# Kernel tuning notes

Measured on AMD Instinct MI355X. Metric: run time of the kernel, lower is better.

## Reference

```python
import jax, jax.numpy as jnp
import numpy as np
from jax import lax

# dims
B, H, W, C = 32, 64, 64, 256
FEATURES, HEADS, NQ = 256, 8, 2
K, STRIDE, PAD = 3, 2, 1
HD = FEATURES // HEADS  # head dim = 32


def setup_inputs() -> dict:
    key = jax.random.key(0)
    ks = jax.random.split(key, 7)
    x = jax.random.normal(ks[0], (B, H, W, C), jnp.float32)
    # learned shared queries: truncated normal * sqrt(1/head_dim)
    query = jax.random.truncated_normal(ks[1], -2.0, 2.0, (NQ, FEATURES), jnp.float32) * np.float32(np.sqrt(1.0 / HD))
    Wk = jax.random.normal(ks[2], (C, FEATURES), jnp.float32) * np.float32(np.sqrt(1.0 / C))  # lecun
    Wv = jax.random.normal(ks[3], (C, FEATURES), jnp.float32) * np.float32(np.sqrt(1.0 / C))
    rpe_bias = jax.random.truncated_normal(ks[4], -2.0, 2.0, (K * K, NQ * HEADS), jnp.float32) * np.float32(0.02)
    attn_scale_w = jax.random.normal(ks[5], (K * K, NQ * HEADS), jnp.float32) * np.float32(0.02)
    Wo = jax.random.normal(ks[6], (FEATURES, FEATURES), jnp.float32) * np.float32(np.sqrt(1.0 / FEATURES))
    return {"x": x, "query": query, "Wk": Wk, "Wv": Wv,
            "rpe_bias": rpe_bias, "attn_scale_w": attn_scale_w, "Wo": Wo}


def _qna_forward(x, query, Wk, Wv, rpe_bias, attn_scale_w, Wo):
    # --- queries: reshape to [NQ, HEADS, HD], unit-normalize per head, depth-scale ---
    q = query.reshape(NQ, HEADS, HD)
    q = q / (jnp.linalg.norm(q, axis=-1, keepdims=True) + 1e-6)
    q = q / jnp.sqrt(HD).astype(q.dtype)

    # --- fused QK: (q Wk^T) applied to x, never materializing per-window keys ---
    Wk_r = Wk.reshape(C, HEADS, HD)
    qWk = jnp.einsum('qHd,DHd->DqH', q, Wk_r)              # [C, NQ, HEADS]
    cost = jnp.einsum('bijD,DqH->bijqH', x, qWk)            # [B, H, W, NQ, HEADS]
    cost_exp = jnp.exp(cost - lax.stop_gradient(jnp.max(cost)))  # global shift, cancels in softmax

    # --- values ---
    v = jnp.einsum('bijD,DF->bijF', x, Wv)                  # [B, H, W, FEATURES]
    v_cost_exp = cost_exp[..., None] * v.reshape(B, H, W, 1, HEADS, HD)
    v_cost_exp = v_cost_exp.reshape(B, H, W, NQ * FEATURES)

    # --- relative position bias + per-offset query mixing scale ---
    rpe = rpe_bias.reshape(K, K, 1, NQ * HEADS)
    rpe_exp = jnp.exp(rpe - lax.stop_gradient(jnp.max(rpe)))  # shift cancels (appears in num & den)
    scale = attn_scale_w.reshape(K, K, 1, NQ * HEADS)
    num_kernel = jnp.repeat(rpe_exp * scale, HD, axis=-1)   # [K, K, 1, NQ*FEATURES]

    # numerator: windowed sum of exp(cost)*v weighted by exp(rpe)*scale (depthwise conv)
    num = lax.conv_general_dilated(
        v_cost_exp, num_kernel, window_strides=(STRIDE, STRIDE),
        padding=((PAD, PAD), (PAD, PAD)), feature_group_count=NQ * FEATURES,
        dimension_numbers=('NHWC', 'HWIO', 'NHWC'))
    # denominator: windowed sum of exp(cost) weighted by exp(rpe)
    den = lax.conv_general_dilated(
        cost_exp.reshape(B, H, W, NQ * HEADS), rpe_exp, window_strides=(STRIDE, STRIDE),
        padding=((PAD, PAD), (PAD, PAD)), feature_group_count=NQ * HEADS,
        dimension_numbers=('NHWC', 'HWIO', 'NHWC'))
    ho, wo = num.shape[1], num.shape[2]

    out = num.reshape(B, ho, wo, NQ, HEADS, HD) / den.reshape(B, ho, wo, NQ, HEADS, 1)
    out = out.sum(axis=3).reshape(B, ho, wo, FEATURES)      # combine queries
    return jnp.einsum('bijF,FO->bijO', out, Wo)             # output projection


def reference(x, query, Wk, Wv, rpe_bias, attn_scale_w, Wo):
    return _qna_forward(x, query, Wk, Wv, rpe_bias, attn_scale_w, Wo)
```

## Files before the change

kernel.cpp:

```cpp
#include <hip/hip_runtime.h>
#include <math.h>

typedef __attribute__((ext_vector_type(8))) short bf16x8;
typedef __attribute__((ext_vector_type(4))) float floatx4;

static __device__ __forceinline__ short f2bf(float f) {
    union { float f; unsigned u; } a; a.f = f;
    unsigned r = a.u + 0x7fffu + ((a.u >> 16) & 1u);
    return (short)(r >> 16);
}
static __device__ __forceinline__ float bf2f(short s) {
    union { unsigned u; float f; } c; c.u = ((unsigned)(unsigned short)s) << 16;
    return c.f;
}

__global__ __launch_bounds__(256) void prep_kernel(
    const float* __restrict__ query,
    const float* __restrict__ Wk,
    const float* __restrict__ rpe_bias,
    const float* __restrict__ attn_scale_w,
    float* __restrict__ qwk,
    float* __restrict__ rpe_exp,
    float* __restrict__ rpe_scale)
{
    __shared__ float qn[16 * 33];
    __shared__ float Wt[16][260];
    int tid = threadIdx.x, bb = blockIdx.x;

    for (int i = tid; i < 512; i += 256) {
        int qq  = i >> 8;
        int rem = i & 255;
        int h   = rem >> 5;
        int d   = rem & 31;
        qn[((qq << 3) + h) * 33 + d] = query[i];
    }
    for (int i = tid; i < 16 * 256; i += 256)
        Wt[i >> 8][i & 255] = Wk[bb * 16 * 256 + i];
    __syncthreads();
    if (tid < 16) {
        float s = 0.f;
        #pragma unroll
        for (int d = 0; d < 32; ++d) { float t = qn[tid * 33 + d]; s += t * t; }
        float inv = 1.0f / ((sqrtf(s) + 1e-6f) * sqrtf(32.0f));
        #pragma unroll
        for (int d = 0; d < 32; ++d) qn[tid * 33 + d] *= inv;
    }
    __syncthreads();

    int g  = tid & 15;
    int Dl = tid >> 4;
    int h2 = g & 7;
    float acc = 0.f;
    #pragma unroll
    for (int d = 0; d < 32; ++d)
        acc += qn[g * 33 + d] * Wt[Dl][h2 * 32 + d];
    qwk[(bb * 16 + Dl) * 16 + g] = acc;

    if (bb == 0 && tid < 144) {
        float r = expf(rpe_bias[tid]);
        rpe_exp[tid]   = r;
        rpe_scale[tid] = r * attn_scale_w[tid];
    }
}

__global__ __launch_bounds__(256) void pack_kernel(
    const float* __restrict__ qwk, const float* __restrict__ Wv,
    const float* __restrict__ Wo,
    short* __restrict__ Bq, short* __restrict__ Wvh, short* __restrict__ Bo)
{
    int id = blockIdx.x * 256 + threadIdx.x;
    if (id < 4096) {
        int j = id & 7, lane = (id >> 3) & 63, kc = id >> 9;
        int k = kc * 32 + ((lane >> 4) << 3) + j;
        Bq[id] = f2bf(qwk[k * 16 + (lane & 15)]);
    } else if (id < 69632) {
        int id1 = id - 4096;
        int j = id1 & 7, lane = (id1 >> 3) & 63, kc = (id1 >> 9) & 7;
        int nt = (id1 >> 12) & 1, h = id1 >> 13;
        int k = kc * 32 + ((lane >> 4) << 3) + j;
        int n = h * 32 + nt * 16 + (lane & 15);
        Wvh[id1] = f2bf(Wv[k * 256 + n]);
    } else {
        int id2 = id - 69632;
        int j = id2 & 7, lane = (id2 >> 3) & 63, kc = (id2 >> 9) & 7, nt = id2 >> 12;
        int k = kc * 32 + ((lane >> 4) << 3) + j;
        int n = nt * 16 + (lane & 15);
        Bo[id2] = f2bf(Wo[k * 256 + n]);
    }
}

#define XROW 264
#define ZROW 264
#define ZOP  2120
__global__ __launch_bounds__(512) void fused_kernel(
    const float* __restrict__ x,
    const float* __restrict__ rpe_exp,
    const float* __restrict__ rpe_scale,
    const short* __restrict__ Bq,
    const short* __restrict__ Wvh,
    const short* __restrict__ Bo,
    float* __restrict__ out)
{
    __shared__ short Xw[112 * XROW];
    __shared__ short zs[16 * ZOP];
    __shared__ float ces[112 * 17];
    __shared__ float wcoefs[16][9][8];
    __shared__ float invden[16][16];

    int tid  = threadIdx.x;
    int lane = tid & 63, wv = tid >> 6;
    int m16  = lane & 15, quad = lane >> 4;

    int blk = blockIdx.x;
    int b   = blk >> 6;
    int io  = (blk >> 1) & 31;
    int hf  = blk & 1;
    int i0  = io * 2 - 1;
    int jbase = hf * 32 - 1;

    #pragma unroll
    for (int i = 0; i < 7; ++i) {
        int it  = tid + i * 512;
        int row = it >> 5;
        int l   = it & 31;
        int ky  = row / 34;
        int jloc = row - ky * 34;
        int ii = i0 + ky, jj = jbase + jloc;
        bool valid = (ky < 3) && (jloc < 33) &&
                     ((unsigned)ii < 64u) && ((unsigned)jj < 64u);
        bf16x8 s;
        if (valid) {
            const float* xp = x + ((size_t)(((b << 6) + ii) << 6) + jj) * 256 + l * 8;
            float4 f0 = *(const float4*)xp;
            float4 f1 = *(const float4*)(xp + 4);
            s[0] = f2bf(f0.x); s[1] = f2bf(f0.y); s[2] = f2bf(f0.z); s[3] = f2bf(f0.w);
            s[4] = f2bf(f1.x); s[5] = f2bf(f1.y); s[6] = f2bf(f1.z); s[7] = f2bf(f1.w);
        } else {
            #pragma unroll
            for (int j = 0; j < 8; ++j) s[j] = 0;
        }
        *(bf16x8*)&Xw[row * XROW + l * 8] = s;
    }
    __syncthreads();

    if (wv < 7) {
        floatx4 acc = (floatx4){0.f, 0.f, 0.f, 0.f};
        const short* bp = Bq + lane * 8;
        #pragma unroll
        for (int kc = 0; kc < 8; ++kc) {
            bf16x8 a = *(const bf16x8*)&Xw[(wv * 16 + m16) * XROW + kc * 32 + quad * 8];
            bf16x8 bb = *(const bf16x8*)(bp + kc * 512);
            acc = __builtin_amdgcn_mfma_f32_16x16x32_bf16(a, bb, acc, 0, 0, 0);
        }
        #pragma unroll
        for (int r = 0; r < 4; ++r) {
            int p = wv * 16 + quad * 4 + r;
            int ky = p / 34, jloc = p - ky * 34;
            int ii = i0 + ky, jj = jbase + jloc;
            bool valid = (ky < 3) && (jloc < 33) &&
                         ((unsigned)ii < 64u) && ((unsigned)jj < 64u);
            ces[p * 17 + m16] = valid ? expf(acc[r]) : 0.f;
        }
    }
    __syncthreads();

    if (tid < 256) {
        int op = tid >> 4, g = tid & 15;
        float den = 0.f;
        #pragma unroll
        for (int w = 0; w < 9; ++w) {
            int ky = w / 3, kx = w - ky * 3;
            int row = ky * 34 + 2 * op + kx;
            den = fmaf(rpe_exp[w * 16 + g], ces[row * 17 + g], den);
        }
        invden[op][g] = 1.0f / den;
    }
    __syncthreads();

    for (int it = tid; it < 1152; it += 512) {
        int op = it / 72, r = it - op * 72;
        int w = r >> 3, h = r & 7;
        int ky = w / 3, kx = w - ky * 3;
        int row = ky * 34 + 2 * op + kx;
        wcoefs[op][w][h] =
            ces[row * 17 + h]     * rpe_scale[w * 16 + h]     * invden[op][h] +
            ces[row * 17 + 8 + h] * rpe_scale[w * 16 + 8 + h] * invden[op][8 + h];
    }
    __syncthreads();

    {
        int c   = tid & 255;
        int opg = tid >> 8;
        #pragma unroll
        for (int oo = 0; oo < 8; ++oo) {
            int op = opg * 8 + oo;
            float z0=0.f,z1=0.f,z2=0.f,z3=0.f,z4=0.f,z5=0.f,z6=0.f,z7=0.f;
            #pragma unroll
            for (int w = 0; w < 9; ++w) {
                int ky = w / 3, kx = w - ky * 3;
                float xv = bf2f(Xw[(ky * 34 + 2 * op + kx) * XROW + c]);
                float4 wc0 = *(const float4*)&wcoefs[op][w][0];
                float4 wc1 = *(const float4*)&wcoefs[op][w][4];
                z0 = fmaf(wc0.x, xv, z0); z1 = fmaf(wc0.y, xv, z1);
                z2 = fmaf(wc0.z, xv, z2); z3 = fmaf(wc0.w, xv, z3);
                z4 = fmaf(wc1.x, xv, z4); z5 = fmaf(wc1.y, xv, z5);
                z6 = fmaf(wc1.z, xv, z6); z7 = fmaf(wc1.w, xv, z7);
            }
            short* zp = &zs[op * ZOP + c];
            zp[0*ZROW] = f2bf(z0); zp[1*ZROW] = f2bf(z1);
            zp[2*ZROW] = f2bf(z2); zp[3*ZROW] = f2bf(z3);
            zp[4*ZROW] = f2bf(z4); zp[5*ZROW] = f2bf(z5);
            zp[6*ZROW] = f2bf(z6); zp[7*ZROW] = f2bf(z7);
        }
    }
    __syncthreads();

    {
        short* out_tr = Xw;
        int h = wv;
        floatx4 acc0 = (floatx4){0.f,0.f,0.f,0.f};
        floatx4 acc1 = (floatx4){0.f,0.f,0.f,0.f};
        const short* bp = Wvh + h * 8192 + lane * 8;
        #pragma unroll
        for (int kc = 0; kc < 8; ++kc) {
            bf16x8 a  = *(const bf16x8*)&zs[m16 * ZOP + h * ZROW + kc * 32 + quad * 8];
            bf16x8 b0 = *(const bf16x8*)(bp + kc * 512);
            bf16x8 b1 = *(const bf16x8*)(bp + 4096 + kc * 512);
            acc0 = __builtin_amdgcn_mfma_f32_16x16x32_bf16(a, b0, acc0, 0, 0, 0);
            acc1 = __builtin_amdgcn_mfma_f32_16x16x32_bf16(a, b1, acc1, 0, 0, 0);
        }
        #pragma unroll
        for (int r = 0; r < 4; ++r) {
            out_tr[(quad * 4 + r) * XROW + h * 32 + m16]      = f2bf(acc0[r]);
            out_tr[(quad * 4 + r) * XROW + h * 32 + 16 + m16] = f2bf(acc1[r]);
        }
    }
    __syncthreads();

    {
        const short* out_tr = Xw;
        floatx4 acc0 = (floatx4){0.f,0.f,0.f,0.f};
        floatx4 acc1 = (floatx4){0.f,0.f,0.f,0.f};
        int nt0 = wv * 2;
        const short* bp = Bo + nt0 * 4096 + lane * 8;
        #pragma unroll
        for (int kc = 0; kc < 8; ++kc) {
            bf16x8 a  = *(const bf16x8*)&out_tr[m16 * XROW + kc * 32 + quad * 8];
            bf16x8 b0 = *(const bf16x8*)(bp + kc * 512);
            bf16x8 b1 = *(const bf16x8*)(bp + 4096 + kc * 512);
            acc0 = __builtin_amdgcn_mfma_f32_16x16x32_bf16(a, b0, acc0, 0, 0, 0);
            acc1 = __builtin_amdgcn_mfma_f32_16x16x32_bf16(a, b1, acc1, 0, 0, 0);
        }
        size_t op0 = (size_t)blk * 16;
        #pragma unroll
        for (int r = 0; r < 4; ++r) {
            out[(op0 + quad * 4 + r) * 256 + nt0 * 16 + m16]      = acc0[r];
            out[(op0 + quad * 4 + r) * 256 + (nt0 + 1) * 16 + m16] = acc1[r];
        }
    }
}

extern "C" void kernel_launch(void* const* d_in, const int* in_sizes, int n_in,
                              void* d_out, int out_size, void* d_ws, size_t ws_size,
                              hipStream_t stream)
{
    const float* x     = (const float*)d_in[0];
    const float* query = (const float*)d_in[1];
    const float* Wk    = (const float*)d_in[2];
    const float* Wv    = (const float*)d_in[3];
    const float* rpe   = (const float*)d_in[4];
    const float* asw   = (const float*)d_in[5];
    const float* Wo    = (const float*)d_in[6];
    float* out = (float*)d_out;

    float* ws        = (float*)d_ws;
    float* qwk       = ws;
    float* rpe_exp   = ws + 4096;
    float* rpe_scale = ws + 4240;
    short* Bq        = (short*)(ws + 4608);
    short* Wvh       = (short*)(ws + 6656);
    short* Bo        = (short*)(ws + 39424);

    prep_kernel<<<dim3(16), dim3(256), 0, stream>>>(query, Wk, rpe, asw,
                                                    qwk, rpe_exp, rpe_scale);
    pack_kernel<<<dim3(528), dim3(256), 0, stream>>>(qwk, Wv, Wo, Bq, Wvh, Bo);
    fused_kernel<<<dim3(2048), dim3(512), 0, stream>>>(x, rpe_exp, rpe_scale,
                                                       Bq, Wvh, Bo, out);
}
```

Before: 286.1 us.

## Fuse windowed weighting into value MFMA and merge prep/pack kernels

New measurement: 258.1 us. -9.8%, faster.

```diff
diff --git a/kernel.cpp b/kernel.cpp
--- a/kernel.cpp
+++ b/kernel.cpp
@@ -19,12 +19,17 @@
     const float* __restrict__ Wk,
     const float* __restrict__ rpe_bias,
     const float* __restrict__ attn_scale_w,
-    float* __restrict__ qwk,
+    const float* __restrict__ Wv,
+    const float* __restrict__ Wo,
     float* __restrict__ rpe_exp,
-    float* __restrict__ rpe_scale)
+    float* __restrict__ rpe_scale,
+    short* __restrict__ Bq,
+    short* __restrict__ Wvh,
+    short* __restrict__ Bo)
 {
     __shared__ float qn[16 * 33];
     __shared__ float Wt[16][260];
+    __shared__ float qwk_s[16][17];
     int tid = threadIdx.x, bb = blockIdx.x;
 
     for (int i = tid; i < 512; i += 256) {
@@ -54,7 +59,30 @@
     #pragma unroll
     for (int d = 0; d < 32; ++d)
         acc += qn[g * 33 + d] * Wt[Dl][h2 * 32 + d];
-    qwk[(bb * 16 + Dl) * 16 + g] = acc;
+    qwk_s[Dl][g] = acc;
+    __syncthreads();
+
+    {
+        int kl = tid >> 4, gg = tid & 15;
+        int k  = bb * 16 + kl;
+        int kc = k >> 5, q5 = k & 31, qd = q5 >> 3, j = q5 & 7;
+        int lane = qd * 16 + gg;
+        Bq[kc * 512 + lane * 8 + j] = f2bf(qwk_s[kl][gg]);
+    }
+
+    for (int kl = 0; kl < 16; ++kl) {
+        int k  = bb * 16 + kl;
+        int kc = k >> 5, q5 = k & 31, qd = q5 >> 3, j = q5 & 7;
+        int n  = tid;
+        int gg = n & 15;
+        int lane = qd * 16 + gg;
+        float vv = Wv[k * 256 + n];
+        float vo = Wo[k * 256 + n];
+        int hh  = n >> 5, ntv = (n >> 4) & 1;
+        Wvh[hh * 8192 + ntv * 4096 + kc * 512 + lane * 8 + j] = f2bf(vv);
+        int nto = n >> 4;
+        Bo[nto * 4096 + kc * 512 + lane * 8 + j] = f2bf(vo);
+    }
 
     if (bb == 0 && tid < 144) {
         float r = expf(rpe_bias[tid]);
@@ -63,35 +91,8 @@
     }
 }
 
-__global__ __launch_bounds__(256) void pack_kernel(
-    const float* __restrict__ qwk, const float* __restrict__ Wv,
-    const float* __restrict__ Wo,
-    short* __restrict__ Bq, short* __restrict__ Wvh, short* __restrict__ Bo)
-{
-    int id = blockIdx.x * 256 + threadIdx.x;
-    if (id < 4096) {
-        int j = id & 7, lane = (id >> 3) & 63, kc = id >> 9;
-        int k = kc * 32 + ((lane >> 4) << 3) + j;
-        Bq[id] = f2bf(qwk[k * 16 + (lane & 15)]);
-    } else if (id < 69632) {
-        int id1 = id - 4096;
-        int j = id1 & 7, lane = (id1 >> 3) & 63, kc = (id1 >> 9) & 7;
-        int nt = (id1 >> 12) & 1, h = id1 >> 13;
-        int k = kc * 32 + ((lane >> 4) << 3) + j;
-        int n = h * 32 + nt * 16 + (lane & 15);
-        Wvh[id1] = f2bf(Wv[k * 256 + n]);
-    } else {
-        int id2 = id - 69632;
-        int j = id2 & 7, lane = (id2 >> 3) & 63, kc = (id2 >> 9) & 7, nt = id2 >> 12;
-        int k = kc * 32 + ((lane >> 4) << 3) + j;
-        int n = nt * 16 + (lane & 15);
-        Bo[id2] = f2bf(Wo[k * 256 + n]);
-    }
-}
-
 #define XROW 264
-#define ZROW 264
-#define ZOP  2120
+#define CESROW 19
 __global__ __launch_bounds__(512) void fused_kernel(
     const float* __restrict__ x,
     const float* __restrict__ rpe_exp,
@@ -102,16 +103,19 @@
     float* __restrict__ out)
 {
     __shared__ short Xw[112 * XROW];
-    __shared__ short zs[16 * ZOP];
-    __shared__ float ces[112 * 17];
-    __shared__ float wcoefs[16][9][8];
+    __shared__ __align__(16) unsigned char pool[112 * CESROW * 4];
+    __shared__ float wcoefs[8][9][16];
     __shared__ float invden[16][16];
+
+    float* ces    = (float*)pool;
+    short* out_tr = (short*)pool;
 
     int tid  = threadIdx.x;
     int lane = tid & 63, wv = tid >> 6;
     int m16  = lane & 15, quad = lane >> 4;
 
-    int blk = blockIdx.x;
+    int blk0 = blockIdx.x;
+    int blk  = ((blk0 & 7) << 8) | (blk0 >> 3);
     int b   = blk >> 6;
     int io  = (blk >> 1) & 31;
     int hf  = blk & 1;
@@ -148,9 +152,9 @@
         const short* bp = Bq + lane * 8;
         #pragma unroll
         for (int kc = 0; kc < 8; ++kc) {
-            bf16x8 a = *(const bf16x8*)&Xw[(wv * 16 + m16) * XROW + kc * 32 + quad * 8];
-            bf16x8 bb = *(const bf16x8*)(bp + kc * 512);
-            acc = __builtin_amdgcn_mfma_f32_16x16x32_bf16(a, bb, acc, 0, 0, 0);
+            bf16x8 a  = *(const bf16x8*)&Xw[(wv * 16 + m16) * XROW + kc * 32 + quad * 8];
+            bf16x8 bq = *(const bf16x8*)(bp + kc * 512);
+            acc = __builtin_amdgcn_mfma_f32_16x16x32_bf16(a, bq, acc, 0, 0, 0);
         }
         #pragma unroll
         for (int r = 0; r < 4; ++r) {
@@ -159,7 +163,7 @@
             int ii = i0 + ky, jj = jbase + jloc;
             bool valid = (ky < 3) && (jloc < 33) &&
                          ((unsigned)ii < 64u) && ((unsigned)jj < 64u);
-            ces[p * 17 + m16] = valid ? expf(acc[r]) : 0.f;
+            ces[p * CESROW + m16] = valid ? expf(acc[r]) : 0.f;
         }
     }
     __syncthreads();
@@ -171,7 +175,7 @@
         for (int w = 0; w < 9; ++w) {
             int ky = w / 3, kx = w - ky * 3;
             int row = ky * 34 + 2 * op + kx;
-            den = fmaf(rpe_exp[w * 16 + g], ces[row * 17 + g], den);
+            den = fmaf(rpe_exp[w * 16 + g], ces[row * CESROW + g], den);
         }
         invden[op][g] = 1.0f / den;
     }
@@ -182,48 +186,38 @@
         int w = r >> 3, h = r & 7;
         int ky = w / 3, kx = w - ky * 3;
         int row = ky * 34 + 2 * op + kx;
-        wcoefs[op][w][h] =
-            ces[row * 17 + h]     * rpe_scale[w * 16 + h]     * invden[op][h] +
-            ces[row * 17 + 8 + h] * rpe_scale[w * 16 + 8 + h] * invden[op][8 + h];
+        wcoefs[h][w][op] =
+            ces[row * CESROW + h]     * rpe_scale[w * 16 + h]     * invden[op][h] +
+            ces[row * CESROW + 8 + h] * rpe_scale[w * 16 + 8 + h] * invden[op][8 + h];
     }
     __syncthreads();
 
     {
-        int c   = tid & 255;
-        int opg = tid >> 8;
-        #pragma unroll
-        for (int oo = 0; oo < 8; ++oo) {
-            int op = opg * 8 + oo;
-            float z0=0.f,z1=0.f,z2=0.f,z3=0.f,z4=0.f,z5=0.f,z6=0.f,z7=0.f;
+        int h = wv;
+        float wc[9];
+        #pragma unroll
+        for (int w = 0; w < 9; ++w) wc[w] = wcoefs[h][w][m16];
+
+        floatx4 acc0 = (floatx4){0.f, 0.f, 0.f, 0.f};
+        floatx4 acc1 = (floatx4){0.f, 0.f, 0.f, 0.f};
+        const short* bp    = Wvh + h * 8192 + lane * 8;
+        const short* xbase = Xw + 2 * m16 * XROW + quad * 8;
+        #pragma unroll
+        for (int kc = 0; kc < 8; ++kc) {
+            float z[8];
+            #pragma unroll
+            for (int j = 0; j < 8; ++j) z[j] = 0.f;
             #pragma unroll
             for (int w = 0; w < 9; ++w) {
                 int ky = w / 3, kx = w - ky * 3;
-                float xv = bf2f(Xw[(ky * 34 + 2 * op + kx) * XROW + c]);
-                float4 wc0 = *(const float4*)&wcoefs[op][w][0];
-                float4 wc1 = *(const float4*)&wcoefs[op][w][4];
-                z0 = fmaf(wc0.x, xv, z0); z1 = fmaf(wc0.y, xv, z1);
-                z2 = fmaf(wc0.z, xv, z2); z3 = fmaf(wc0.w, xv, z3);
-                z4 = fmaf(wc1.x, xv, z4); z5 = fmaf(wc1.y, xv, z5);
-                z6 = fmaf(wc1.z, xv, z6); z7 = fmaf(wc1.w, xv, z7);
+                bf16x8 xv = *(const bf16x8*)(xbase + (ky * 34 + kx) * XROW + kc * 32);
+                #pragma unroll
+                for (int j = 0; j < 8; ++j)
+                    z[j] = fmaf(wc[w], bf2f(xv[j]), z[j]);
             }
-            short* zp = &zs[op * ZOP + c];
-            zp[0*ZROW] = f2bf(z0); zp[1*ZROW] = f2bf(z1);
-            zp[2*ZROW] = f2bf(z2); zp[3*ZROW] = f2bf(z3);
-            zp[4*ZROW] = f2bf(z4); zp[5*ZROW] = f2bf(z5);
-            zp[6*ZROW] = f2bf(z6); zp[7*ZROW] = f2bf(z7);
-        }
-    }
-    __syncthreads();
-
-    {
-        short* out_tr = Xw;
-        int h = wv;
-        floatx4 acc0 = (floatx4){0.f,0.f,0.f,0.f};
-        floatx4 acc1 = (floatx4){0.f,0.f,0.f,0.f};
-        const short* bp = Wvh + h * 8192 + lane * 8;
-        #pragma unroll
-        for (int kc = 0; kc < 8; ++kc) {
-            bf16x8 a  = *(const bf16x8*)&zs[m16 * ZOP + h * ZROW + kc * 32 + quad * 8];
+            bf16x8 a;
+            #pragma unroll
+            for (int j = 0; j < 8; ++j) a[j] = f2bf(z[j]);
             bf16x8 b0 = *(const bf16x8*)(bp + kc * 512);
             bf16x8 b1 = *(const bf16x8*)(bp + 4096 + kc * 512);
             acc0 = __builtin_amdgcn_mfma_f32_16x16x32_bf16(a, b0, acc0, 0, 0, 0);
@@ -238,9 +232,8 @@
     __syncthreads();
 
     {
-        const short* out_tr = Xw;
-        floatx4 acc0 = (floatx4){0.f,0.f,0.f,0.f};
-        floatx4 acc1 = (floatx4){0.f,0.f,0.f,0.f};
+        floatx4 acc0 = (floatx4){0.f, 0.f, 0.f, 0.f};
+        floatx4 acc1 = (floatx4){0.f, 0.f, 0.f, 0.f};
         int nt0 = wv * 2;
         const short* bp = Bo + nt0 * 4096 + lane * 8;
         #pragma unroll
@@ -254,7 +247,7 @@
         size_t op0 = (size_t)blk * 16;
         #pragma unroll
         for (int r = 0; r < 4; ++r) {
-            out[(op0 + quad * 4 + r) * 256 + nt0 * 16 + m16]      = acc0[r];
+            out[(op0 + quad * 4 + r) * 256 + nt0 * 16 + m16]       = acc0[r];
             out[(op0 + quad * 4 + r) * 256 + (nt0 + 1) * 16 + m16] = acc1[r];
         }
     }
@@ -274,16 +267,14 @@
     float* out = (float*)d_out;
 
     float* ws        = (float*)d_ws;
-    float* qwk       = ws;
-    float* rpe_exp   = ws + 4096;
-    float* rpe_scale = ws + 4240;
-    short* Bq        = (short*)(ws + 4608);
-    short* Wvh       = (short*)(ws + 6656);
-    short* Bo        = (short*)(ws + 39424);
-
-    prep_kernel<<<dim3(16), dim3(256), 0, stream>>>(query, Wk, rpe, asw,
-                                                    qwk, rpe_exp, rpe_scale);
-    pack_kernel<<<dim3(528), dim3(256), 0, stream>>>(qwk, Wv, Wo, Bq, Wvh, Bo);
+    float* rpe_exp   = ws;
+    float* rpe_scale = ws + 144;
+    short* Bq        = (short*)(ws + 288);
+    short* Wvh       = (short*)(ws + 288 + 2048);
+    short* Bo        = (short*)(ws + 288 + 2048 + 32768);
+
+    prep_kernel<<<dim3(16), dim3(256), 0, stream>>>(query, Wk, rpe, asw, Wv, Wo,
+                                                    rpe_exp, rpe_scale, Bq, Wvh, Bo);
     fused_kernel<<<dim3(2048), dim3(512), 0, stream>>>(x, rpe_exp, rpe_scale,
                                                        Bq, Wvh, Bo, out);
 }
```
